# Performance work log

Measured on AMD Instinct MI355X. Metric: run time of the kernel, lower is better.

## Reference

```python
import jax, jax.numpy as jnp
import numpy as np

D = 512; NH = 8; NL = 6; DFF = 2048
TOK = 1024; APP = 3; V = TOK + APP; PAD = V - 1
B = 256; SENC = 16; LTGT = 62


def setup_inputs() -> dict:
    key = jax.random.key(0)
    ks = jax.random.split(key, 14)
    g = lambda k, shp, s=0.02: jax.random.normal(k, shp, jnp.float32) * s
    return dict(
        encoder_out=jax.random.normal(ks[0], (B, SENC, D), jnp.float32),
        point_out=jax.random.normal(ks[1], (B, D), jnp.float32),
        emb=g(ks[2], (V, D)),
        pos_embed=g(ks[3], (1, LTGT, D)),
        sa_inw=g(ks[4], (NL, 3 * D, D)), sa_inb=jnp.zeros((NL, 3 * D), jnp.float32),
        sa_outw=g(ks[5], (NL, D, D)), sa_outb=jnp.zeros((NL, D), jnp.float32),
        ca_inw=g(ks[6], (NL, 3 * D, D)), ca_inb=jnp.zeros((NL, 3 * D), jnp.float32),
        ca_outw=g(ks[7], (NL, D, D)), ca_outb=jnp.zeros((NL, D), jnp.float32),
        ln1_s=jnp.ones((NL, D), jnp.float32), ln1_b=jnp.zeros((NL, D), jnp.float32),
        ln2_s=jnp.ones((NL, D), jnp.float32), ln2_b=jnp.zeros((NL, D), jnp.float32),
        ln3_s=jnp.ones((NL, D), jnp.float32), ln3_b=jnp.zeros((NL, D), jnp.float32),
        ff1_w=g(ks[8], (NL, DFF, D)), ff1_b=jnp.zeros((NL, DFF), jnp.float32),
        ff2_w=g(ks[9], (NL, D, DFF)), ff2_b=jnp.zeros((NL, D), jnp.float32),
        out_w=g(ks[10], (V, D)), out_b=jnp.zeros((V,), jnp.float32),
        tgt=jax.random.randint(ks[11], (B, LTGT), 0, TOK),
    )


def _ln(x, s, b, eps=1e-5):
    m = x.mean(-1, keepdims=True)
    v = ((x - m) ** 2).mean(-1, keepdims=True)
    return (x - m) / jnp.sqrt(v + eps) * s + b


def _mha(q_in, kv_in, inw, inb, outw, outb, mask):
    # PyTorch MultiheadAttention with packed in_proj [3D, D]
    hd = D // NH
    wq, wk, wv = inw[:D], inw[D:2 * D], inw[2 * D:]
    bq, bk, bv = inb[:D], inb[D:2 * D], inb[2 * D:]
    Bq, Tq = q_in.shape[0], q_in.shape[1]
    Tk = kv_in.shape[1]
    q = (q_in @ wq.T + bq).reshape(Bq, Tq, NH, hd)
    k = (kv_in @ wk.T + bk).reshape(Bq, Tk, NH, hd)
    v = (kv_in @ wv.T + bv).reshape(Bq, Tk, NH, hd)
    s = jnp.einsum('bqhd,bkhd->bhqk', q, k) / np.float32(np.sqrt(hd))
    if mask is not None:
        s = s + mask
    a = jax.nn.softmax(s, axis=-1)
    o = jnp.einsum('bhqk,bkhd->bqhd', a, v).reshape(Bq, Tq, D)
    return o @ outw.T + outb


def reference(encoder_out, point_out, emb, pos_embed,
              sa_inw, sa_inb, sa_outw, sa_outb,
              ca_inw, ca_inb, ca_outw, ca_outb,
              ln1_s, ln1_b, ln2_s, ln2_b, ln3_s, ln3_b,
              ff1_w, ff1_b, ff2_w, ff2_b, out_w, out_b, tgt):
    # scheduled_sampling_ratio == 1.0 => the per-step loop always writes the
    # ground-truth token, so output_sequence == tgt[:, :-1] and the returned
    # tensor equals one full causal decoder pass over tgt[:, :-1].
    tokens = tgt[:, :-1]                      # [B, L], L = 61
    L = tokens.shape[1]
    neg = jnp.float32(-jnp.inf)
    causal = jnp.where(jnp.triu(jnp.ones((L, L), bool), 1), neg, 0.0)
    padm = jnp.where(tokens == PAD, neg, 0.0)[:, None, None, :]  # [B,1,1,L]
    mask = causal[None, None] + padm          # [B,1,L,L]
    mem = encoder_out[:, :1, :]               # memory length 1 (encoder_out[:, [0]])
    x = emb[tokens] + point_out[:, None, :] + pos_embed[0, :L]
    for i in range(NL):
        x = _ln(x + _mha(x, x, sa_inw[i], sa_inb[i], sa_outw[i], sa_outb[i], mask), ln1_s[i], ln1_b[i])
        x = _ln(x + _mha(x, mem, ca_inw[i], ca_inb[i], ca_outw[i], ca_outb[i], None), ln2_s[i], ln2_b[i])
        h = jax.nn.relu(x @ ff1_w[i].T + ff1_b[i]) @ ff2_w[i].T + ff2_b[i]
        x = _ln(x + h, ln3_s[i], ln3_b[i])
    return x @ out_w.T + out_b               # [B, L, V]
```

## Files before the change

### kernel.cpp

```cpp
#include <hip/hip_runtime.h>
#include <stdint.h>
#include <stddef.h>

typedef unsigned short u16;
typedef float f4 __attribute__((ext_vector_type(4)));
typedef float f32x4 __attribute__((ext_vector_type(4)));
typedef short bf16x8 __attribute__((ext_vector_type(8)));
typedef u16 u16x4 __attribute__((ext_vector_type(4)));
typedef int i4v __attribute__((ext_vector_type(4)));

#define PAD_TOK 1026
#define LQ 61
#define NBATCH 256
#define MTOT (NBATCH * LQ)

__device__ __forceinline__ u16 f2b(float f) {
  uint32_t x = __float_as_uint(f);
  x += 0x7fff + ((x >> 16) & 1);
  return (u16)(x >> 16);
}
__device__ __forceinline__ float b2f(u16 u) {
  return __uint_as_float(((uint32_t)u) << 16);
}

#define GLDS(gptr, lptr) __builtin_amdgcn_global_load_lds( \
    (const __attribute__((address_space(1))) void*)(gptr), \
    (__attribute__((address_space(3))) void*)(lptr), 16, 0, 0)

__device__ __forceinline__ bf16x8 ldfrag(const u16* buf, int row, int ksl, int kg) {
  const int chunk = (ksl * 4 + kg) ^ (row & 7);
  return *(const bf16x8*)&buf[row * 64 + chunk * 8];
}

__global__ __launch_bounds__(512) void gemm_bt2(
    const u16* __restrict__ A, const u16* __restrict__ W,
    const float* __restrict__ bias,
    float* __restrict__ Cf, u16* __restrict__ Cb,
    int N, int K, int Nreal, int ldc, int relu)
{
  __shared__ u16 SH[384 * 64];
  u16* const As = SH;
  u16* const Bs = SH + 8192;

  const int gx = gridDim.x;
  const int nwg = gx * gridDim.y;
  const int orig = blockIdx.y * gx + blockIdx.x;
  const int q8 = nwg >> 3, r8 = nwg & 7;
  const int xcd = orig & 7, off = orig >> 3;
  const int nid = (xcd < r8 ? xcd * (q8 + 1) : r8 * (q8 + 1) + (xcd - r8) * q8) + off;
  const int bx = nid % gx, by = nid / gx;

  const int tid = threadIdx.x;
  const int wid = tid >> 6, lane = tid & 63;
  const int wm = wid >> 2, wn = wid & 3;
  const long m0 = (long)by * 128;
  const long n0 = (long)bx * 256;

  const int lr = lane >> 3;
  const int lc = lane & 7;
  const int scol = ((lc ^ lr) << 3);

  f32x4 acc[4][4];
#pragma unroll
  for (int i = 0; i < 4; ++i)
#pragma unroll
    for (int j = 0; j < 4; ++j) acc[i][j] = (f32x4){0.f, 0.f, 0.f, 0.f};

  const u16* Abase = A + m0 * K;
  const u16* Wbase = W + n0 * K;
  const int r = lane & 15, kg = lane >> 4;

  for (int kt = 0; kt < K; kt += 64) {
#pragma unroll
    for (int c = 0; c < 2; ++c) {
      const int row = wid * 16 + c * 8;
      GLDS(Abase + (long)(row + lr) * K + kt + scol, &As[row * 64]);
    }
#pragma unroll
    for (int c = 0; c < 4; ++c) {
      const int row = wid * 32 + c * 8;
      GLDS(Wbase + (long)(row + lr) * K + kt + scol, &Bs[row * 64]);
    }
    __syncthreads();

#pragma unroll
    for (int ks = 0; ks < 2; ++ks) {
      bf16x8 a[4], b[4];
#pragma unroll
      for (int mi = 0; mi < 4; ++mi)
        a[mi] = ldfrag(As, wm * 64 + mi * 16 + r, ks, kg);
#pragma unroll
      for (int ni = 0; ni < 4; ++ni)
        b[ni] = ldfrag(Bs, wn * 64 + ni * 16 + r, ks, kg);
#pragma unroll
      for (int mi = 0; mi < 4; ++mi)
#pragma unroll
        for (int ni = 0; ni < 4; ++ni)
          acc[mi][ni] = __builtin_amdgcn_mfma_f32_16x16x32_bf16(a[mi], b[ni], acc[mi][ni], 0, 0, 0);
    }
    __syncthreads();
  }

  const int cr4 = (lane >> 4) * 4;
  const int cc = lane & 15;

  if (Cb) {
#pragma unroll
    for (int half = 0; half < 2; ++half) {
      if (wm == half) {
#pragma unroll
        for (int ni = 0; ni < 4; ++ni) {
          const int coll = wn * 64 + ni * 16 + cc;
          const float bv = bias[(int)n0 + coll];
#pragma unroll
          for (int mi = 0; mi < 4; ++mi) {
#pragma unroll
            for (int j = 0; j < 4; ++j) {
              const int rowl = mi * 16 + cr4 + j;
              float v = acc[mi][ni][j] + bv;
              if (relu) v = fmaxf(v, 0.f);
              const int phys = (coll >> 3) ^ (rowl & 31);
              SH[rowl * 256 + phys * 8 + (coll & 7)] = f2b(v);
            }
          }
        }
      }
      __syncthreads();
#pragma unroll
      for (int i = 0; i < 4; ++i) {
        const int t = i * 512 + tid;
        const int row = t >> 5, ch = t & 31;
        const int n = (int)n0 + ch * 8;
        if (n < Nreal) {
          const int phys = ch ^ (row & 31);
          *(bf16x8*)&Cb[(m0 + half * 64 + row) * (long)N + n] =
              *(const bf16x8*)&SH[row * 256 + phys * 8];
        }
      }
      __syncthreads();
    }
  } else {
#pragma unroll
    for (int ni = 0; ni < 4; ++ni) {
      const int n = (int)n0 + wn * 64 + ni * 16 + cc;
      if (n >= Nreal) continue;
      const float bv = bias[n];
#pragma unroll
      for (int mi = 0; mi < 4; ++mi) {
#pragma unroll
        for (int j = 0; j < 4; ++j) {
          const long m = m0 + wm * 64 + mi * 16 + cr4 + j;
          float v = acc[mi][ni][j] + bv;
          if (relu) v = fmaxf(v, 0.f);
          Cf[m * ldc + n] = v;
        }
      }
    }
  }
}

template<int BM>
__global__ __launch_bounds__(256) void gemm_bt(
    const u16* __restrict__ A, const u16* __restrict__ W,
    const float* __restrict__ bias,
    float* __restrict__ Cf, u16* __restrict__ Cb,
    int M, int N, int K, int Nreal, int ldc, int relu,
    long aZ, long wZ, long bZ, long cZ)
{
  constexpr int MI = BM / 32;
  const int z = blockIdx.z;
  A += z * aZ; W += z * wZ; bias += z * bZ;
  if (Cf) Cf += z * cZ;
  if (Cb) Cb += z * cZ;

  __shared__ u16 As[BM * 64];
  __shared__ u16 Bs[128 * 64];

  const int gx = gridDim.x;
  const int nwg = gx * gridDim.y;
  const int orig = blockIdx.y * gx + blockIdx.x;
  const int q8 = nwg >> 3, r8 = nwg & 7;
  const int xcd = orig & 7, off = orig >> 3;
  const int nid = (xcd < r8 ? xcd * (q8 + 1) : r8 * (q8 + 1) + (xcd - r8) * q8) + off;
  const int bx = nid % gx, by = nid / gx;

  const int tid = threadIdx.x;
  const int wid = tid >> 6, lane = tid & 63;
  const int wr = wid >> 1, wc = wid & 1;
  const long m0 = (long)by * BM;
  const long n0 = (long)bx * 128;

  const int lr = lane >> 3;
  const int lc = lane & 7;
  const int scol = ((lc ^ lr) << 3);

  f32x4 acc[MI][4];
#pragma unroll
  for (int i = 0; i < MI; ++i)
#pragma unroll
    for (int j = 0; j < 4; ++j) acc[i][j] = (f32x4){0.f, 0.f, 0.f, 0.f};

  const u16* Abase = A + m0 * K;
  const u16* Wbase = W + n0 * K;
  const int r = lane & 15, kg = lane >> 4;

  for (int kt = 0; kt < K; kt += 64) {
#pragma unroll
    for (int c = 0; c < BM / 32; ++c) {
      const int row = wid * (BM / 4) + c * 8;
      GLDS(Abase + (long)(row + lr) * K + kt + scol, &As[row * 64]);
    }
#pragma unroll
    for (int c = 0; c < 4; ++c) {
      const int row = wid * 32 + c * 8;
      GLDS(Wbase + (long)(row + lr) * K + kt + scol, &Bs[row * 64]);
    }
    __syncthreads();

#pragma unroll
    for (int ks = 0; ks < 2; ++ks) {
      bf16x8 a[MI], b[4];
#pragma unroll
      for (int mi = 0; mi < MI; ++mi)
        a[mi] = ldfrag(As, wr * (BM / 2) + mi * 16 + r, ks, kg);
#pragma unroll
      for (int ni = 0; ni < 4; ++ni)
        b[ni] = ldfrag(Bs, wc * 64 + ni * 16 + r, ks, kg);
#pragma unroll
      for (int mi = 0; mi < MI; ++mi)
#pragma unroll
        for (int ni = 0; ni < 4; ++ni)
          acc[mi][ni] = __builtin_amdgcn_mfma_f32_16x16x32_bf16(a[mi], b[ni], acc[mi][ni], 0, 0, 0);
    }
    __syncthreads();
  }

  const int cr4 = (lane >> 4) * 4;
  const int cc = lane & 15;

  if (Cb) {
#pragma unroll
    for (int ni = 0; ni < 4; ++ni) {
      const int coll = wc * 64 + ni * 16 + cc;
      const float bv = bias[(int)n0 + coll];
#pragma unroll
      for (int mi = 0; mi < MI; ++mi) {
#pragma unroll
        for (int j = 0; j < 4; ++j) {
          const int rowl = wr * (BM / 2) + mi * 16 + cr4 + j;
          float v = acc[mi][ni][j] + bv;
          if (relu) v = fmaxf(v, 0.f);
          const int sw = (rowl & 7) << 3;
          u16* half = (coll & 64) ? Bs : As;
          half[rowl * 64 + ((coll & 63) ^ sw)] = f2b(v);
        }
      }
    }
    __syncthreads();
    constexpr int PT = BM / 16;
#pragma unroll
    for (int i = 0; i < PT; ++i) {
      const int t = i * 256 + tid;
      const int row = t >> 4, ch = t & 15;
      const int n = (int)n0 + ch * 8;
      if (n < Nreal) {
        const int phys = (ch & 7) ^ (row & 7);
        const u16* half = (ch < 8) ? As : Bs;
        bf16x8 vv = *(const bf16x8*)&half[row * 64 + phys * 8];
        *(bf16x8*)&Cb[(m0 + row) * (long)N + n] = vv;
      }
    }
  } else {
#pragma unroll
    for (int ni = 0; ni < 4; ++ni) {
      const int n = (int)n0 + wc * 64 + ni * 16 + cc;
      if (n >= Nreal) continue;
      const float bv = bias[n];
#pragma unroll
      for (int mi = 0; mi < MI; ++mi) {
#pragma unroll
        for (int j = 0; j < 4; ++j) {
          const long m = m0 + wr * (BM / 2) + mi * 16 + cr4 + j;
          float v = acc[mi][ni][j] + bv;
          if (relu) v = fmaxf(v, 0.f);
          Cf[m * ldc + n] = v;
        }
      }
    }
  }
}

__global__ __launch_bounds__(512) void gemmln_k(
    const u16* __restrict__ A, const u16* __restrict__ W,
    const float* __restrict__ bias,
    const u16* __restrict__ cavb,
    const float* __restrict__ s1w, const float* __restrict__ b1w,
    const float* __restrict__ s2w, const float* __restrict__ b2w,
    u16* __restrict__ XB, int K)
{
  __shared__ u16 LDSBUF[2][36864];
  __shared__ float LSTAT[64][8];
  __shared__ u16 LCAV[1536];
  u16* const EP = &LDSBUF[0][0];

  const int nwg = gridDim.x;
  const int orig = blockIdx.x;
  const int q8 = nwg >> 3, r8 = nwg & 7;
  const int xcd = orig & 7, off = orig >> 3;
  const int by = (xcd < r8 ? xcd * (q8 + 1) : r8 * (q8 + 1) + (xcd - r8) * q8) + off;

  const int tid = threadIdx.x;
  const int wid = tid >> 6, lane = tid & 63;
  const int wm = wid >> 2, wn = wid & 3;
  const long m0 = (long)by * 64;

  const int lr = lane >> 3, lc = lane & 7;
  const int scol = ((lc ^ lr) << 3);
  const int r = lane & 15, kg = lane >> 4;

  f32x4 acc[2][8];
#pragma unroll
  for (int i = 0; i < 2; ++i)
#pragma unroll
    for (int j = 0; j < 8; ++j) acc[i][j] = (f32x4){0.f, 0.f, 0.f, 0.f};

  const u16* Abase = A + m0 * K;

#define STAGE(buf, kt) do {                                              \
    const int arow_ = wid * 8;                                           \
    GLDS(Abase + (long)(arow_ + lr) * K + (kt) + scol,                   \
         &(buf)[32768 + arow_ * 64]);                                    \
    _Pragma("unroll")                                                    \
    for (int c_ = 0; c_ < 8; ++c_) {                                     \
      const int row_ = wid * 64 + c_ * 8;                                \
      GLDS(W + (long)(row_ + lr) * K + (kt) + scol, &(buf)[row_ * 64]);  \
    }                                                                    \
  } while (0)

  const int nt = K >> 6;
  STAGE(LDSBUF[0], 0);
  asm volatile("s_waitcnt vmcnt(0)" ::: "memory");
  __builtin_amdgcn_sched_barrier(0);
  __builtin_amdgcn_s_barrier();

  for (int t = 0; t < nt; ++t) {
    u16* const bufc = &LDSBUF[t & 1][0];
    if (t + 1 < nt) STAGE(LDSBUF[(t + 1) & 1], (t + 1) << 6);
#pragma unroll
    for (int ks = 0; ks < 2; ++ks) {
      bf16x8 a0 = ldfrag(bufc + 32768, wm * 32 + r, ks, kg);
      bf16x8 a1 = ldfrag(bufc + 32768, wm * 32 + 16 + r, ks, kg);
      __builtin_amdgcn_s_setprio(1);
#pragma unroll
      for (int ni = 0; ni < 8; ++ni) {
        bf16x8 b = ldfrag(bufc, wn * 128 + ni * 16 + r, ks, kg);
        acc[0][ni] = __builtin_amdgcn_mfma_f32_16x16x32_bf16(a0, b, acc[0][ni], 0, 0, 0);
        acc[1][ni] = __builtin_amdgcn_mfma_f32_16x16x32_bf16(a1, b, acc[1][ni], 0, 0, 0);
      }
      __builtin_amdgcn_s_setprio(0);
    }
    asm volatile("s_waitcnt vmcnt(0)" ::: "memory");
    __builtin_amdgcn_sched_barrier(0);
    __builtin_amdgcn_s_barrier();
  }
#undef STAGE

  const int b0 = (int)(m0 / LQ);
  const int bsplit1 = (b0 + 1) * LQ;
  const int bsplit2 = (b0 + 2) * LQ;

#pragma unroll
  for (int i = 0; i < 8; ++i) {
    const int t = i * 512 + tid;
    const int row = t >> 6, ch = t & 63;
    *(bf16x8*)&EP[row * 516 + ch * 8] =
        *(const bf16x8*)&XB[(m0 + row) * 512 + ch * 8];
  }
  for (int t = tid; t < 1536; t += 512) {
    const int bb = t >> 9, c = t & 511;
    int bi = b0 + bb;
    if (bi > NBATCH - 1) bi = NBATCH - 1;
    LCAV[bb * 512 + c] = cavb[(long)bi * 512 + c];
  }
  __syncthreads();

  float bcol[8];
#pragma unroll
  for (int ni = 0; ni < 8; ++ni) bcol[ni] = bias[wn * 128 + ni * 16 + r];
#pragma unroll
  for (int mi = 0; mi < 2; ++mi)
#pragma unroll
    for (int ni = 0; ni < 8; ++ni) {
      const int col = wn * 128 + ni * 16 + r;
#pragma unroll
      for (int j = 0; j < 4; ++j) {
        const int row = wm * 32 + mi * 16 + kg * 4 + j;
        acc[mi][ni][j] += bcol[ni] + b2f(EP[row * 516 + col]);
      }
    }

#pragma unroll
  for (int mi = 0; mi < 2; ++mi)
#pragma unroll
    for (int j = 0; j < 4; ++j) {
      float s1 = 0.f, s2 = 0.f;
#pragma unroll
      for (int ni = 0; ni < 8; ++ni) {
        const float v = acc[mi][ni][j];
        s1 += v; s2 += v * v;
      }
#pragma unroll
      for (int o = 1; o < 16; o <<= 1) {
        s1 += __shfl_xor(s1, o);
        s2 += __shfl_xor(s2, o);
      }
      if (r == 0) {
        const int row = wm * 32 + mi * 16 + kg * 4 + j;
        LSTAT[row][wn] = s1;
        LSTAT[row][4 + wn] = s2;
      }
    }
  __syncthreads();

  float sc[8], bc[8];
#pragma unroll
  for (int ni = 0; ni < 8; ++ni) {
    const int col = wn * 128 + ni * 16 + r;
    sc[ni] = s1w[col]; bc[ni] = b1w[col];
  }
#pragma unroll
  for (int mi = 0; mi < 2; ++mi)
#pragma unroll
    for (int j = 0; j < 4; ++j) {
      const int row = wm * 32 + mi * 16 + kg * 4 + j;
      const float S1 = LSTAT[row][0] + LSTAT[row][1] + LSTAT[row][2] + LSTAT[row][3];
      const float S2 = LSTAT[row][4] + LSTAT[row][5] + LSTAT[row][6] + LSTAT[row][7];
      const float mean = S1 * (1.f / 512.f);
      const float var = S2 * (1.f / 512.f) - mean * mean;
      const float rstd = rsqrtf(var + 1e-5f);
#pragma unroll
      for (int ni = 0; ni < 8; ++ni)
        acc[mi][ni][j] = (acc[mi][ni][j] - mean) * rstd * sc[ni] + bc[ni];
    }

#pragma unroll
  for (int mi = 0; mi < 2; ++mi)
#pragma unroll
    for (int j = 0; j < 4; ++j) {
      const int row = wm * 32 + mi * 16 + kg * 4 + j;
      const int gr = (int)m0 + row;
      const int sel = (gr >= bsplit2) ? 2 : ((gr >= bsplit1) ? 1 : 0);
#pragma unroll
      for (int ni = 0; ni < 8; ++ni) {
        const int col = wn * 128 + ni * 16 + r;
        acc[mi][ni][j] += b2f(LCAV[sel * 512 + col]);
      }
    }
  __syncthreads();
#pragma unroll
  for (int mi = 0; mi < 2; ++mi)
#pragma unroll
    for (int j = 0; j < 4; ++j) {
      float s1 = 0.f, s2 = 0.f;
#pragma unroll
      for (int ni = 0; ni < 8; ++ni) {
        const float v = acc[mi][ni][j];
        s1 += v; s2 += v * v;
      }
#pragma unroll
      for (int o = 1; o < 16; o <<= 1) {
        s1 += __shfl_xor(s1, o);
        s2 += __shfl_xor(s2, o);
      }
      if (r == 0) {
        const int row = wm * 32 + mi * 16 + kg * 4 + j;
        LSTAT[row][wn] = s1;
        LSTAT[row][4 + wn] = s2;
      }
    }
  __syncthreads();
#pragma unroll
  for (int ni = 0; ni < 8; ++ni) {
    const int col = wn * 128 + ni * 16 + r;
    sc[ni] = s2w[col]; bc[ni] = b2w[col];
  }
#pragma unroll
  for (int mi = 0; mi < 2; ++mi)
#pragma unroll
    for (int j = 0; j < 4; ++j) {
      const int row = wm * 32 + mi * 16 + kg * 4 + j;
      const float S1 = LSTAT[row][0] + LSTAT[row][1] + LSTAT[row][2] + LSTAT[row][3];
      const float S2 = LSTAT[row][4] + LSTAT[row][5] + LSTAT[row][6] + LSTAT[row][7];
      const float mean = S1 * (1.f / 512.f);
      const float var = S2 * (1.f / 512.f) - mean * mean;
      const float rstd = rsqrtf(var + 1e-5f);
#pragma unroll
      for (int ni = 0; ni < 8; ++ni)
        acc[mi][ni][j] = (acc[mi][ni][j] - mean) * rstd * sc[ni] + bc[ni];
    }

#pragma unroll
  for (int mi = 0; mi < 2; ++mi)
#pragma unroll
    for (int ni = 0; ni < 8; ++ni) {
      const int col = wn * 128 + ni * 16 + r;
#pragma unroll
      for (int j = 0; j < 4; ++j) {
        const int row = wm * 32 + mi * 16 + kg * 4 + j;
        EP[row * 516 + col] = f2b(acc[mi][ni][j]);
      }
    }
  __syncthreads();
#pragma unroll
  for (int i = 0; i < 8; ++i) {
    const int t = i * 512 + tid;
    const int row = t >> 6, ch = t & 63;
    *(bf16x8*)&XB[(m0 + row) * 512 + ch * 8] =
        *(const bf16x8*)&EP[row * 516 + ch * 8];
  }
}

__global__ __launch_bounds__(256) void attn_k(const u16* __restrict__ qkv,
                                              const int* __restrict__ tgt,
                                              u16* __restrict__ outp)
{
  __shared__ u16 Qs[64 * 72];
  __shared__ u16 Ks[64 * 72];
  __shared__ u16 Vt[64 * 72];
  __shared__ float S[64 * 65];
  __shared__ int stok[64];

  const int bid = blockIdx.x;
  const int b = bid >> 3, h = bid & 7;
  const int tid = threadIdx.x;
  const int tr = tid >> 2, seg = tid & 3;

  if (tid < 64) stok[tid] = (tid < 61) ? tgt[b * 62 + tid] : -1;

  const long rowbase = ((long)(b * LQ + tr)) * 1536 + h * 64;
  if (tr < LQ) {
    const i4v* qsrc = (const i4v*)(qkv + rowbase + seg * 16);
    i4v q0 = qsrc[0], q1 = qsrc[1];
    *(i4v*)&Qs[tr * 72 + seg * 16] = q0;
    *(i4v*)&Qs[tr * 72 + seg * 16 + 8] = q1;
    const i4v* ksrc = (const i4v*)(qkv + rowbase + 512 + seg * 16);
    i4v k0 = ksrc[0], k1 = ksrc[1];
    *(i4v*)&Ks[tr * 72 + seg * 16] = k0;
    *(i4v*)&Ks[tr * 72 + seg * 16 + 8] = k1;
    const u16* vsrc = qkv + rowbase + 1024 + seg * 16;
#pragma unroll
    for (int i = 0; i < 16; ++i) Vt[(seg * 16 + i) * 72 + tr] = vsrc[i];
  } else {
    i4v zz = {0, 0, 0, 0};
    *(i4v*)&Qs[tr * 72 + seg * 16] = zz;
    *(i4v*)&Qs[tr * 72 + seg * 16 + 8] = zz;
    *(i4v*)&Ks[tr * 72 + seg * 16] = zz;
    *(i4v*)&Ks[tr * 72 + seg * 16 + 8] = zz;
#pragma unroll
    for (int i = 0; i < 16; ++i) Vt[(seg * 16 + i) * 72 + tr] = 0;
  }
  __syncthreads();

  const int lane = tid & 63, w = tid >> 6;
  const int r = lane & 15, kg = lane >> 4;

  {
    f32x4 s[4];
#pragma unroll
    for (int ni = 0; ni < 4; ++ni) s[ni] = (f32x4){0.f, 0.f, 0.f, 0.f};
    bf16x8 a0 = *(const bf16x8*)&Qs[(w * 16 + r) * 72 + kg * 8];
    bf16x8 a1 = *(const bf16x8*)&Qs[(w * 16 + r) * 72 + 32 + kg * 8];
#pragma unroll
    for (int ni = 0; ni < 4; ++ni) {
      bf16x8 b0 = *(const bf16x8*)&Ks[(ni * 16 + r) * 72 + kg * 8];
      bf16x8 b1 = *(const bf16x8*)&Ks[(ni * 16 + r) * 72 + 32 + kg * 8];
      s[ni] = __builtin_amdgcn_mfma_f32_16x16x32_bf16(a0, b0, s[ni], 0, 0, 0);
      s[ni] = __builtin_amdgcn_mfma_f32_16x16x32_bf16(a1, b1, s[ni], 0, 0, 0);
    }
#pragma unroll
    for (int ni = 0; ni < 4; ++ni)
#pragma unroll
      for (int j = 0; j < 4; ++j)
        S[(w * 16 + kg * 4 + j) * 65 + ni * 16 + r] = s[ni][j];
  }
  __syncthreads();

  {
    const int row = tid >> 2, g = tid & 3;
    float vals[16];
    float mx = -3e38f;
#pragma unroll
    for (int i = 0; i < 16; ++i) {
      const int k = g * 16 + i;
      float v = S[row * 65 + k] * 0.125f;
      const bool ok = (k <= row) && (k < LQ) && (stok[k] != PAD_TOK);
      v = ok ? v : -1e30f;
      vals[i] = v;
      mx = fmaxf(mx, v);
    }
    mx = fmaxf(mx, __shfl_xor(mx, 1));
    mx = fmaxf(mx, __shfl_xor(mx, 2));
    float sum = 0.f;
#pragma unroll
    for (int i = 0; i < 16; ++i) { float e = __expf(vals[i] - mx); vals[i] = e; sum += e; }
    sum += __shfl_xor(sum, 1);
    sum += __shfl_xor(sum, 2);
    const float inv = 1.f / sum;
#pragma unroll
    for (int i = 0; i < 16; ++i) Qs[row * 72 + g * 16 + i] = f2b(vals[i] * inv);
  }
  __syncthreads();

  {
    f32x4 o[4];
#pragma unroll
    for (int ni = 0; ni < 4; ++ni) o[ni] = (f32x4){0.f, 0.f, 0.f, 0.f};
    bf16x8 a0 = *(const bf16x8*)&Qs[(w * 16 + r) * 72 + kg * 8];
    bf16x8 a1 = *(const bf16x8*)&Qs[(w * 16 + r) * 72 + 32 + kg * 8];
#pragma unroll
    for (int ni = 0; ni < 4; ++ni) {
      bf16x8 b0 = *(const bf16x8*)&Vt[(ni * 16 + r) * 72 + kg * 8];
      bf16x8 b1 = *(const bf16x8*)&Vt[(ni * 16 + r) * 72 + 32 + kg * 8];
      o[ni] = __builtin_amdgcn_mfma_f32_16x16x32_bf16(a0, b0, o[ni], 0, 0, 0);
      o[ni] = __builtin_amdgcn_mfma_f32_16x16x32_bf16(a1, b1, o[ni], 0, 0, 0);
    }
#pragma unroll
    for (int ni = 0; ni < 4; ++ni)
#pragma unroll
      for (int j = 0; j < 4; ++j) {
        const int qrow = w * 16 + kg * 4 + j;
        const int col = ni * 16 + r;
        Ks[qrow * 64 + (col ^ ((qrow & 7) << 3))] = f2b(o[ni][j]);
      }
  }
  __syncthreads();

  {
    const int row = tid >> 2, sub = tid & 3;
    if (row < LQ) {
      const long obase = ((long)(b * LQ + row)) * 512 + h * 64;
#pragma unroll
      for (int i = 0; i < 2; ++i) {
        const int ch = i * 4 + sub;
        const int phys = ch ^ (row & 7);
        bf16x8 vv = *(const bf16x8*)&Ks[row * 64 + phys * 8];
        *(bf16x8*)&outp[obase + ch * 8] = vv;
      }
    }
  }
}

__device__ __forceinline__ void ln_row(f4& v0, f4& v1,
                                       const float* __restrict__ sw,
                                       const float* __restrict__ bw, int d0) {
  float s1 = v0[0] + v0[1] + v0[2] + v0[3] + v1[0] + v1[1] + v1[2] + v1[3];
  float s2 = v0[0]*v0[0] + v0[1]*v0[1] + v0[2]*v0[2] + v0[3]*v0[3]
           + v1[0]*v1[0] + v1[1]*v1[1] + v1[2]*v1[2] + v1[3]*v1[3];
#pragma unroll
  for (int off = 1; off < 64; off <<= 1) {
    s1 += __shfl_xor(s1, off);
    s2 += __shfl_xor(s2, off);
  }
  const float mean = s1 * (1.f / 512.f);
  const float var = s2 * (1.f / 512.f) - mean * mean;
  const float rstd = rsqrtf(var + 1e-5f);
  const f4* sp = (const f4*)(sw + d0);
  const f4* bp = (const f4*)(bw + d0);
  f4 ss0 = sp[0], ss1 = sp[1], bb0 = bp[0], bb1 = bp[1];
#pragma unroll
  for (int i = 0; i < 4; ++i) {
    v0[i] = (v0[i] - mean) * rstd * ss0[i] + bb0[i];
    v1[i] = (v1[i] - mean) * rstd * ss1[i] + bb1[i];
  }
}

__global__ __launch_bounds__(256) void lnf3_k(const u16* __restrict__ p,
                                              const u16* __restrict__ xr,
                                              const float* __restrict__ s1,
                                              const float* __restrict__ b1,
                                              u16* __restrict__ out)
{
  const int m = blockIdx.x * 4 + (threadIdx.x >> 6);
  const int lane = threadIdx.x & 63;
  const int d0 = lane * 8;
  bf16x8 pv = *(const bf16x8*)(p + (long)m * 512 + d0);
  bf16x8 xv = *(const bf16x8*)(xr + (long)m * 512 + d0);
  f4 v0, v1;
#pragma unroll
  for (int i = 0; i < 4; ++i) {
    v0[i] = b2f((u16)pv[i]) + b2f((u16)xv[i]);
    v1[i] = b2f((u16)pv[4 + i]) + b2f((u16)xv[4 + i]);
  }
  ln_row(v0, v1, s1, b1, d0);
  u16x4* ob = (u16x4*)(out + (long)m * 512 + d0);
  ob[0] = (u16x4){f2b(v0[0]), f2b(v0[1]), f2b(v0[2]), f2b(v0[3])};
  ob[1] = (u16x4){f2b(v1[0]), f2b(v1[1]), f2b(v1[2]), f2b(v1[3])};
}

__global__ __launch_bounds__(256) void embed_k(const float* __restrict__ emb,
                                               const float* __restrict__ pout,
                                               const float* __restrict__ pos,
                                               const int* __restrict__ tgt,
                                               u16* __restrict__ XB)
{
  const int m = blockIdx.x * 4 + (threadIdx.x >> 6);
  const int lane = threadIdx.x & 63;
  const int b = m / LQ, t = m % LQ;
  const int tok = tgt[b * 62 + t];
  const int d0 = lane * 8;
  const f4* e = (const f4*)(emb + (long)tok * 512 + d0);
  const f4* p = (const f4*)(pout + (long)b * 512 + d0);
  const f4* q = (const f4*)(pos + (long)t * 512 + d0);
  f4 v0 = e[0] + p[0] + q[0];
  f4 v1 = e[1] + p[1] + q[1];
  u16x4* xb = (u16x4*)(XB + (long)m * 512 + d0);
  xb[0] = (u16x4){f2b(v0[0]), f2b(v0[1]), f2b(v0[2]), f2b(v0[3])};
  xb[1] = (u16x4){f2b(v1[0]), f2b(v1[1]), f2b(v1[2]), f2b(v1[3])};
}

__global__ void cvtall_k(const float* __restrict__ s0, const float* __restrict__ s1,
                         const float* __restrict__ s2, const float* __restrict__ s3,
                         const float* __restrict__ s4,
                         u16* __restrict__ d0, u16* __restrict__ d1,
                         u16* __restrict__ d2, u16* __restrict__ d3,
                         u16* __restrict__ d4)
{
  const int N0 = 1179648;
  const int N1 = N0 + 393216;
  const int N2 = N1 + 393216;
  const int N3 = N2 + 1572864;
  const int N4 = N3 + 1572864;
  for (int i = blockIdx.x * 256 + threadIdx.x; i < N4; i += gridDim.x * 256) {
    const float* s; u16* d; int k;
    if (i < N0)      { s = s0; d = d0; k = i; }
    else if (i < N1) { s = s1; d = d1; k = i - N0; }
    else if (i < N2) { s = s2; d = d2; k = i - N1; }
    else if (i < N3) { s = s3; d = d3; k = i - N2; }
    else             { s = s4; d = d4; k = i - N3; }
    f4 v = ((const f4*)s)[k];
    ((u16x4*)d)[k] = (u16x4){f2b(v[0]), f2b(v[1]), f2b(v[2]), f2b(v[3])};
  }
}

__global__ void cvt_ca_v_k(const float* __restrict__ ca_inw, u16* __restrict__ dst) {
  const int i = blockIdx.x * 256 + threadIdx.x;
  if (i >= 393216) return;
  const int l = i >> 16, rem = i & 65535;
  f4 v = ((const f4*)ca_inw)[l * 196608 + 131072 + rem];
  ((u16x4*)dst)[i] = (u16x4){f2b(v[0]), f2b(v[1]), f2b(v[2]), f2b(v[3])};
}

__global__ void cvt_outw_k(const float* __restrict__ out_w, u16* __restrict__ dst) {
  const int i = blockIdx.x * 256 + threadIdx.x;
  if (i >= 163840) return;
  const int row = (i * 4) >> 9;
  u16x4 o = {0, 0, 0, 0};
  if (row < 1027) {
    f4 v = ((const f4*)out_w)[i];
    o = (u16x4){f2b(v[0]), f2b(v[1]), f2b(v[2]), f2b(v[3])};
  }
  ((u16x4*)dst)[i] = o;
}

__global__ void cvt_outb_k(const float* __restrict__ out_b, float* __restrict__ dst) {
  const int i = blockIdx.x * 256 + threadIdx.x;
  if (i >= 1280) return;
  dst[i] = (i < 1027) ? out_b[i] : 0.f;
}

__global__ void cvt_memb_k(const float* __restrict__ enc, u16* __restrict__ dst) {
  const int i = blockIdx.x * 256 + threadIdx.x;
  if (i >= 32768) return;
  const int b = (i * 4) >> 9, d = (i * 4) & 511;
  f4 v = ((const f4*)enc)[(b * 8192 + d) >> 2];
  ((u16x4*)dst)[i] = (u16x4){f2b(v[0]), f2b(v[1]), f2b(v[2]), f2b(v[3])};
}

static constexpr size_t XB_OFF    = 0;
static constexpr size_t P_OFF     = 15990784;
static constexpr size_t BIG_OFF   = 31981568;
static constexpr size_t ATT_OFF   = 95944704;
static constexpr size_t WSA_OFF   = 111935488;
static constexpr size_t WSO_OFF   = 121372672;
static constexpr size_t WCAV_OFF  = 124518400;
static constexpr size_t WCO_OFF   = 127664128;
static constexpr size_t WF1_OFF   = 130809856;
static constexpr size_t WF2_OFF   = 143392768;
static constexpr size_t WOUT_OFF  = 155975680;
static constexpr size_t BOUT_OFF  = 157286400;
static constexpr size_t MEMB_OFF  = 157291520;
static constexpr size_t CATMP_OFF = 157553664;
static constexpr size_t CAVB_OFF  = 159126528;

extern "C" void kernel_launch(void* const* d_in, const int* in_sizes, int n_in,
                              void* d_out, int out_size, void* d_ws, size_t ws_size,
                              hipStream_t stream) {
  (void)in_sizes; (void)n_in; (void)out_size; (void)ws_size;
  const float* encoder_out = (const float*)d_in[0];
  const float* point_out   = (const float*)d_in[1];
  const float* emb         = (const float*)d_in[2];
  const float* pos         = (const float*)d_in[3];
  const float* sa_inw      = (const float*)d_in[4];
  const float* sa_inb      = (const float*)d_in[5];
  const float* sa_outw     = (const float*)d_in[6];
  const float* sa_outb     = (const float*)d_in[7];
  const float* ca_inw      = (const float*)d_in[8];
  const float* ca_inb      = (const float*)d_in[9];
  const float* ca_outw     = (const float*)d_in[10];
  const float* ca_outb     = (const float*)d_in[11];
  const float* ln1_s       = (const float*)d_in[12];
  const float* ln1_b       = (const float*)d_in[13];
  const float* ln2_s       = (const float*)d_in[14];
  const float* ln2_b       = (const float*)d_in[15];
  const float* ln3_s       = (const float*)d_in[16];
  const float* ln3_b       = (const float*)d_in[17];
  const float* ff1_w       = (const float*)d_in[18];
  const float* ff1_b       = (const float*)d_in[19];
  const float* ff2_w       = (const float*)d_in[20];
  const float* ff2_b       = (const float*)d_in[21];
  const float* out_w       = (const float*)d_in[22];
  const float* out_b       = (const float*)d_in[23];
  const int*   tgt         = (const int*)d_in[24];

  char* ws = (char*)d_ws;
  u16*   XB    = (u16*)(ws + XB_OFF);
  u16*   P     = (u16*)(ws + P_OFF);
  u16*   BIG   = (u16*)(ws + BIG_OFF);
  u16*   ATT   = (u16*)(ws + ATT_OFF);
  u16*   WSA   = (u16*)(ws + WSA_OFF);
  u16*   WSO   = (u16*)(ws + WSO_OFF);
  u16*   WCAV  = (u16*)(ws + WCAV_OFF);
  u16*   WCO   = (u16*)(ws + WCO_OFF);
  u16*   WF1   = (u16*)(ws + WF1_OFF);
  u16*   WF2   = (u16*)(ws + WF2_OFF);
  u16*   WOUT  = (u16*)(ws + WOUT_OFF);
  float* BOUT  = (float*)(ws + BOUT_OFF);
  u16*   MEMB  = (u16*)(ws + MEMB_OFF);
  u16*   CATMP = (u16*)(ws + CATMP_OFF);
  u16*   CAVB  = (u16*)(ws + CAVB_OFF);

  cvtall_k<<<dim3(2048), dim3(256), 0, stream>>>(
      sa_inw, sa_outw, ca_outw, ff1_w, ff2_w, WSA, WSO, WCO, WF1, WF2);
  cvt_ca_v_k<<<dim3(1536), dim3(256), 0, stream>>>(ca_inw, WCAV);
  cvt_outw_k<<<dim3(640), dim3(256), 0, stream>>>(out_w, WOUT);
  cvt_outb_k<<<dim3(5), dim3(256), 0, stream>>>(out_b, BOUT);
  cvt_memb_k<<<dim3(128), dim3(256), 0, stream>>>(encoder_out, MEMB);

  embed_k<<<dim3(MTOT / 4), dim3(256), 0, stream>>>(emb, point_out, pos, tgt, XB);

  gemm_bt<64><<<dim3(4, 4, 6), dim3(256), 0, stream>>>(
      MEMB, WCAV, ca_inb + 1024, nullptr, CATMP,
      256, 512, 512, 512, 512, 0,
      0L, 262144L, 1536L, 131072L);
  gemm_bt<64><<<dim3(4, 4, 6), dim3(256), 0, stream>>>(
      CATMP, WCO, ca_outb, nullptr, CAVB,
      256, 512, 512, 512, 512, 0,
      131072L, 262144L, 512L, 131072L);

  for (int l = 0; l < 6; ++l) {
    gemm_bt2<<<dim3(6, 122), dim3(512), 0, stream>>>(
        XB, WSA + (long)l * 786432, sa_inb + l * 1536, nullptr, BIG,
        1536, 512, 1536, 1536, 0);
    attn_k<<<dim3(2048), dim3(256), 0, stream>>>(BIG, tgt, ATT);
    gemmln_k<<<dim3(244), dim3(512), 0, stream>>>(
        ATT, WSO + (long)l * 262144, sa_outb + l * 512,
        CAVB + (long)l * 131072,
        ln1_s + l * 512, ln1_b + l * 512, ln2_s + l * 512, ln2_b + l * 512,
        XB, 512);
    gemm_bt2<<<dim3(8, 122), dim3(512), 0, stream>>>(
        XB, WF1 + (long)l * 1048576, ff1_b + l * 2048, nullptr, BIG,
        2048, 512, 2048, 2048, 1);
    gemm_bt<64><<<dim3(4, 244, 1), dim3(256), 0, stream>>>(
        BIG, WF2 + (long)l * 1048576, ff2_b + l * 512, nullptr, P,
        MTOT, 512, 2048, 512, 512, 0, 0L, 0L, 0L, 0L);
    lnf3_k<<<dim3(MTOT / 4), dim3(256), 0, stream>>>(
        P, XB, ln3_s + l * 512, ln3_b + l * 512, XB);
  }

  gemm_bt2<<<dim3(5, 122), dim3(512), 0, stream>>>(
      XB, WOUT, BOUT, (float*)d_out, nullptr,
      1280, 512, 1027, 1027, 0);
}
```

Baseline: 1.124 ms.

## Add 64x256 FF2 GEMM kernel, stage fp32 epilogue through LDS, merge conversion kernels

Replaces the FF2 GEMM (K=2048, N=512) with a new 512-thread kernel using 64x256 tiles, XCD-aware block remapping and an LDS-staged bf16 epilogue, so each block reuses A over wider N. Rewrites the fp32 output path of gemm_bt2 to stage accumulators through shared memory and write contiguous row chunks, for better-coalesced stores to the final logits. Merges five weight/bias conversion kernels into one launch to cut launch overhead. The new FF2 kernel has no double buffering and a single sync-heavy K loop, so latency hiding may be weaker.

```diff
diff --git a/kernel.cpp b/kernel.cpp
--- a/kernel.cpp
+++ b/kernel.cpp
@@ -21,6 +21,9 @@
 }
 __device__ __forceinline__ float b2f(u16 u) {
   return __uint_as_float(((uint32_t)u) << 16);
+}
+__device__ __forceinline__ u16x4 cvt4(f4 v) {
+  return (u16x4){f2b(v[0]), f2b(v[1]), f2b(v[2]), f2b(v[3])};
 }
 
 #define GLDS(gptr, lptr) __builtin_amdgcn_global_load_lds( \
@@ -140,22 +143,137 @@
       __syncthreads();
     }
   } else {
-#pragma unroll
-    for (int ni = 0; ni < 4; ++ni) {
-      const int n = (int)n0 + wn * 64 + ni * 16 + cc;
-      if (n >= Nreal) continue;
-      const float bv = bias[n];
-#pragma unroll
-      for (int mi = 0; mi < 4; ++mi) {
-#pragma unroll
-        for (int j = 0; j < 4; ++j) {
-          const long m = m0 + wm * 64 + mi * 16 + cr4 + j;
-          float v = acc[mi][ni][j] + bv;
-          if (relu) v = fmaxf(v, 0.f);
-          Cf[m * ldc + n] = v;
+    float* SHf = (float*)SH;
+#pragma unroll
+    for (int q = 0; q < 4; ++q) {
+      if (wm == (q >> 1)) {
+        const int mib = (q & 1) * 2;
+#pragma unroll
+        for (int ni = 0; ni < 4; ++ni) {
+          const int coll = wn * 64 + ni * 16 + cc;
+          const float bv = bias[(int)n0 + coll];
+#pragma unroll
+          for (int mi2 = 0; mi2 < 2; ++mi2) {
+#pragma unroll
+            for (int j = 0; j < 4; ++j) {
+              const int rowl = mi2 * 16 + cr4 + j;
+              float v = acc[mib + mi2][ni][j] + bv;
+              if (relu) v = fmaxf(v, 0.f);
+              SHf[rowl * 260 + coll] = v;
+            }
+          }
         }
       }
-    }
+      __syncthreads();
+      {
+        const int row = tid >> 4, c = tid & 15;
+        const int nbase = (int)n0 + c * 16;
+        const long gro = (m0 + q * 32 + row) * (long)ldc;
+        if (nbase + 16 <= Nreal) {
+#pragma unroll
+          for (int e = 0; e < 16; ++e)
+            Cf[gro + nbase + e] = SHf[row * 260 + c * 16 + e];
+        } else if (nbase < Nreal) {
+          for (int e = 0; e < Nreal - nbase; ++e)
+            Cf[gro + nbase + e] = SHf[row * 260 + c * 16 + e];
+        }
+      }
+      __syncthreads();
+    }
+  }
+}
+
+__global__ __launch_bounds__(512) void gemm_bt3(
+    const u16* __restrict__ A, const u16* __restrict__ W,
+    const float* __restrict__ bias, u16* __restrict__ Cb,
+    int N, int K, int relu)
+{
+  __shared__ u16 SH[320 * 64];
+  u16* const As = SH;
+  u16* const Bs = SH + 4096;
+
+  const int gx = gridDim.x;
+  const int nwg = gx * gridDim.y;
+  const int orig = blockIdx.y * gx + blockIdx.x;
+  const int q8 = nwg >> 3, r8 = nwg & 7;
+  const int xcd = orig & 7, off = orig >> 3;
+  const int nid = (xcd < r8 ? xcd * (q8 + 1) : r8 * (q8 + 1) + (xcd - r8) * q8) + off;
+  const int bx = nid % gx, by = nid / gx;
+
+  const int tid = threadIdx.x;
+  const int wid = tid >> 6, lane = tid & 63;
+  const int wm = wid >> 2, wn = wid & 3;
+  const long m0 = (long)by * 64;
+  const long n0 = (long)bx * 256;
+
+  const int lr = lane >> 3;
+  const int lc = lane & 7;
+  const int scol = ((lc ^ lr) << 3);
+
+  f32x4 acc[2][4];
+#pragma unroll
+  for (int i = 0; i < 2; ++i)
+#pragma unroll
+    for (int j = 0; j < 4; ++j) acc[i][j] = (f32x4){0.f, 0.f, 0.f, 0.f};
+
+  const u16* Abase = A + m0 * K;
+  const u16* Wbase = W + n0 * K;
+  const int r = lane & 15, kg = lane >> 4;
+
+  for (int kt = 0; kt < K; kt += 64) {
+    {
+      const int arow = wid * 8;
+      GLDS(Abase + (long)(arow + lr) * K + kt + scol, &As[arow * 64]);
+#pragma unroll
+      for (int c = 0; c < 4; ++c) {
+        const int row = wid * 32 + c * 8;
+        GLDS(Wbase + (long)(row + lr) * K + kt + scol, &Bs[row * 64]);
+      }
+    }
+    __syncthreads();
+
+#pragma unroll
+    for (int ks = 0; ks < 2; ++ks) {
+      bf16x8 a0 = ldfrag(As, wm * 32 + r, ks, kg);
+      bf16x8 a1 = ldfrag(As, wm * 32 + 16 + r, ks, kg);
+#pragma unroll
+      for (int ni = 0; ni < 4; ++ni) {
+        bf16x8 b = ldfrag(Bs, wn * 64 + ni * 16 + r, ks, kg);
+        acc[0][ni] = __builtin_amdgcn_mfma_f32_16x16x32_bf16(a0, b, acc[0][ni], 0, 0, 0);
+        acc[1][ni] = __builtin_amdgcn_mfma_f32_16x16x32_bf16(a1, b, acc[1][ni], 0, 0, 0);
+      }
+    }
+    __syncthreads();
+  }
+
+  const int cr4 = (lane >> 4) * 4;
+  const int cc = lane & 15;
+
+#pragma unroll
+  for (int ni = 0; ni < 4; ++ni) {
+    const int coll = wn * 64 + ni * 16 + cc;
+    const float bv = bias[(int)n0 + coll];
+#pragma unroll
+    for (int mi = 0; mi < 2; ++mi) {
+#pragma unroll
+      for (int j = 0; j < 4; ++j) {
+        const int rowl = wm * 32 + mi * 16 + cr4 + j;
+        float v = acc[mi][ni][j] + bv;
+        if (relu) v = fmaxf(v, 0.f);
+        const int phys = (coll >> 3) ^ (rowl & 31);
+        SH[rowl * 256 + phys * 8 + (coll & 7)] = f2b(v);
+      }
+    }
+  }
+  __syncthreads();
+#pragma unroll
+  for (int i = 0; i < 4; ++i) {
+    const int t = i * 512 + tid;
+    const int row = t >> 5, ch = t & 31;
+    const int n = (int)n0 + ch * 8;
+    const int phys = ch ^ (row & 31);
+    *(bf16x8*)&Cb[(m0 + row) * (long)N + n] =
+        *(const bf16x8*)&SH[row * 256 + phys * 8];
   }
 }
 
@@ -693,8 +811,8 @@
   }
   ln_row(v0, v1, s1, b1, d0);
   u16x4* ob = (u16x4*)(out + (long)m * 512 + d0);
-  ob[0] = (u16x4){f2b(v0[0]), f2b(v0[1]), f2b(v0[2]), f2b(v0[3])};
-  ob[1] = (u16x4){f2b(v1[0]), f2b(v1[1]), f2b(v1[2]), f2b(v1[3])};
+  ob[0] = cvt4(v0);
+  ob[1] = cvt4(v1);
 }
 
 __global__ __launch_bounds__(256) void embed_k(const float* __restrict__ emb,
@@ -714,66 +832,63 @@
   f4 v0 = e[0] + p[0] + q[0];
   f4 v1 = e[1] + p[1] + q[1];
   u16x4* xb = (u16x4*)(XB + (long)m * 512 + d0);
-  xb[0] = (u16x4){f2b(v0[0]), f2b(v0[1]), f2b(v0[2]), f2b(v0[3])};
-  xb[1] = (u16x4){f2b(v1[0]), f2b(v1[1]), f2b(v1[2]), f2b(v1[3])};
-}
-
-__global__ void cvtall_k(const float* __restrict__ s0, const float* __restrict__ s1,
-                         const float* __restrict__ s2, const float* __restrict__ s3,
-                         const float* __restrict__ s4,
-                         u16* __restrict__ d0, u16* __restrict__ d1,
-                         u16* __restrict__ d2, u16* __restrict__ d3,
-                         u16* __restrict__ d4)
+  xb[0] = cvt4(v0);
+  xb[1] = cvt4(v1);
+}
+
+__global__ void cvtall_k(const float* __restrict__ sa_inw, const float* __restrict__ sa_outw,
+                         const float* __restrict__ ca_outw, const float* __restrict__ ff1_w,
+                         const float* __restrict__ ff2_w, const float* __restrict__ ca_inw,
+                         const float* __restrict__ out_w, const float* __restrict__ out_b,
+                         const float* __restrict__ enc,
+                         u16* __restrict__ WSA, u16* __restrict__ WSO,
+                         u16* __restrict__ WCO, u16* __restrict__ WF1,
+                         u16* __restrict__ WF2, u16* __restrict__ WCAV,
+                         u16* __restrict__ WOUT, float* __restrict__ BOUT,
+                         u16* __restrict__ MEMB)
 {
-  const int N0 = 1179648;
-  const int N1 = N0 + 393216;
-  const int N2 = N1 + 393216;
-  const int N3 = N2 + 1572864;
-  const int N4 = N3 + 1572864;
-  for (int i = blockIdx.x * 256 + threadIdx.x; i < N4; i += gridDim.x * 256) {
-    const float* s; u16* d; int k;
-    if (i < N0)      { s = s0; d = d0; k = i; }
-    else if (i < N1) { s = s1; d = d1; k = i - N0; }
-    else if (i < N2) { s = s2; d = d2; k = i - N1; }
-    else if (i < N3) { s = s3; d = d3; k = i - N2; }
-    else             { s = s4; d = d4; k = i - N3; }
-    f4 v = ((const f4*)s)[k];
-    ((u16x4*)d)[k] = (u16x4){f2b(v[0]), f2b(v[1]), f2b(v[2]), f2b(v[3])};
-  }
-}
-
-__global__ void cvt_ca_v_k(const float* __restrict__ ca_inw, u16* __restrict__ dst) {
-  const int i = blockIdx.x * 256 + threadIdx.x;
-  if (i >= 393216) return;
-  const int l = i >> 16, rem = i & 65535;
-  f4 v = ((const f4*)ca_inw)[l * 196608 + 131072 + rem];
-  ((u16x4*)dst)[i] = (u16x4){f2b(v[0]), f2b(v[1]), f2b(v[2]), f2b(v[3])};
-}
-
-__global__ void cvt_outw_k(const float* __restrict__ out_w, u16* __restrict__ dst) {
-  const int i = blockIdx.x * 256 + threadIdx.x;
-  if (i >= 163840) return;
-  const int row = (i * 4) >> 9;
-  u16x4 o = {0, 0, 0, 0};
-  if (row < 1027) {
-    f4 v = ((const f4*)out_w)[i];
-    o = (u16x4){f2b(v[0]), f2b(v[1]), f2b(v[2]), f2b(v[3])};
-  }
-  ((u16x4*)dst)[i] = o;
-}
-
-__global__ void cvt_outb_k(const float* __restrict__ out_b, float* __restrict__ dst) {
-  const int i = blockIdx.x * 256 + threadIdx.x;
-  if (i >= 1280) return;
-  dst[i] = (i < 1027) ? out_b[i] : 0.f;
-}
-
-__global__ void cvt_memb_k(const float* __restrict__ enc, u16* __restrict__ dst) {
-  const int i = blockIdx.x * 256 + threadIdx.x;
-  if (i >= 32768) return;
-  const int b = (i * 4) >> 9, d = (i * 4) & 511;
-  f4 v = ((const f4*)enc)[(b * 8192 + d) >> 2];
-  ((u16x4*)dst)[i] = (u16x4){f2b(v[0]), f2b(v[1]), f2b(v[2]), f2b(v[3])};
+  const int C0 = 320;
+  const int C1 = C0 + 32768;
+  const int C2 = C1 + 163840;
+  const int C3 = C2 + 393216;
+  const int C4 = C3 + 1179648;
+  const int C5 = C4 + 393216;
+  const int C6 = C5 + 393216;
+  const int C7 = C6 + 1572864;
+  const int C8 = C7 + 1572864;
+  for (int i = blockIdx.x * 256 + threadIdx.x; i < C8; i += gridDim.x * 256) {
+    if (i < C0) {
+      const int base = i * 4;
+#pragma unroll
+      for (int e = 0; e < 4; ++e)
+        BOUT[base + e] = (base + e < 1027) ? out_b[base + e] : 0.f;
+    } else if (i < C1) {
+      const int k = i - C0;
+      const int b = (k * 4) >> 9, d = (k * 4) & 511;
+      f4 v = ((const f4*)enc)[(b * 8192 + d) >> 2];
+      ((u16x4*)MEMB)[k] = cvt4(v);
+    } else if (i < C2) {
+      const int k = i - C1;
+      const int row = (k * 4) >> 9;
+      u16x4 o = {0, 0, 0, 0};
+      if (row < 1027) { f4 v = ((const f4*)out_w)[k]; o = cvt4(v); }
+      ((u16x4*)WOUT)[k] = o;
+    } else if (i < C3) {
+      const int k = i - C2;
+      const int l = k >> 16, rem = k & 65535;
+      f4 v = ((const f4*)ca_inw)[l * 196608 + 131072 + rem];
+      ((u16x4*)WCAV)[k] = cvt4(v);
+    } else {
+      const float* s; u16* d; int k;
+      if (i < C4)      { s = sa_inw;  d = WSA; k = i - C3; }
+      else if (i < C5) { s = sa_outw; d = WSO; k = i - C4; }
+      else if (i < C6) { s = ca_outw; d = WCO; k = i - C5; }
+      else if (i < C7) { s = ff1_w;   d = WF1; k = i - C6; }
+      else             { s = ff2_w;   d = WF2; k = i - C7; }
+      f4 v = ((const f4*)s)[k];
+      ((u16x4*)d)[k] = cvt4(v);
+    }
+  }
 }
 
 static constexpr size_t XB_OFF    = 0;
@@ -840,11 +955,8 @@
   u16*   CAVB  = (u16*)(ws + CAVB_OFF);
 
   cvtall_k<<<dim3(2048), dim3(256), 0, stream>>>(
-      sa_inw, sa_outw, ca_outw, ff1_w, ff2_w, WSA, WSO, WCO, WF1, WF2);
-  cvt_ca_v_k<<<dim3(1536), dim3(256), 0, stream>>>(ca_inw, WCAV);
-  cvt_outw_k<<<dim3(640), dim3(256), 0, stream>>>(out_w, WOUT);
-  cvt_outb_k<<<dim3(5), dim3(256), 0, stream>>>(out_b, BOUT);
-  cvt_memb_k<<<dim3(128), dim3(256), 0, stream>>>(encoder_out, MEMB);
+      sa_inw, sa_outw, ca_outw, ff1_w, ff2_w, ca_inw, out_w, out_b, encoder_out,
+      WSA, WSO, WCO, WF1, WF2, WCAV, WOUT, BOUT, MEMB);
 
   embed_k<<<dim3(MTOT / 4), dim3(256), 0, stream>>>(emb, point_out, pos, tgt, XB);
 
@@ -870,9 +982,9 @@
     gemm_bt2<<<dim3(8, 122), dim3(512), 0, stream>>>(
         XB, WF1 + (long)l * 1048576, ff1_b + l * 2048, nullptr, BIG,
         2048, 512, 2048, 2048, 1);
-    gemm_bt<64><<<dim3(4, 244, 1), dim3(256), 0, stream>>>(
-        BIG, WF2 + (long)l * 1048576, ff2_b + l * 512, nullptr, P,
-        MTOT, 512, 2048, 512, 512, 0, 0L, 0L, 0L, 0L);
+    gemm_bt3<<<dim3(2, 244), dim3(512), 0, stream>>>(
+        BIG, WF2 + (long)l * 1048576, ff2_b + l * 512, P,
+        512, 2048, 0);
     lnf3_k<<<dim3(MTOT / 4), dim3(256), 0, stream>>>(
         P, XB, ln3_s + l * 512, ln3_b + l * 512, XB);
   }
```

Result: no change. 1.110 ms (median of 2 runs) (-1.3%).
